# Kernel optimization log

Measured on AMD Instinct MI355X. Metric: run time of the kernel, lower is better.

The kernel has to match this reference:

```python
import jax, jax.numpy as jnp
import numpy as np

B, S, N, IN_D = 16, 12, 2048, 2
H, HEADS, DH = 64, 4, 16
E = 32768
DT = 0.1            # encoder_scale * seq_in / (encoder_interval*seq_in) steps
STEPS = 12          # encoder_interval * seq_in
NEG_SLOPE = 0.2


def setup_inputs() -> dict:
    key = jax.random.key(0)
    ks = jax.random.split(key, 12)
    s = 1.0 / np.sqrt(H)
    return {
        "inputs": jax.random.normal(ks[0], (B, S, N, IN_D), jnp.float32),
        "w_in": jax.random.normal(ks[1], (IN_D, H), jnp.float32) / np.sqrt(IN_D),
        "b_in": jnp.zeros((H,), jnp.float32),
        "Wh": jax.random.normal(ks[2], (H, H), jnp.float32) * s,
        "bias_g": jnp.zeros((H,), jnp.float32),
        "a_src": jax.random.normal(ks[3], (HEADS, DH), jnp.float32) * s,
        "a_dst": jax.random.normal(ks[4], (HEADS, DH), jnp.float32) * s,
        "w1": jax.random.normal(ks[5], (H, H), jnp.float32) * s,
        "b1": jnp.zeros((H,), jnp.float32),
        "w2": jax.random.normal(ks[6], (H, H), jnp.float32) * s,
        "b2": jnp.zeros((H,), jnp.float32),
        "src": jax.random.randint(ks[7], (E,), 0, N, jnp.int32),
        "dst": jax.random.randint(ks[8], (E,), 0, N, jnp.int32),
    }


def _gat(y, Wh, bias_g, a_src, a_dst, src, dst):
    """Single-layer multi-head GAT: dy/dt. y: [B,N,H]."""
    h = (y @ Wh).reshape(B, N, HEADS, DH)                      # [B,N,h,d]
    e_s = jnp.einsum('bnhd,hd->bnh', h, a_src)                 # [B,N,h]
    e_d = jnp.einsum('bnhd,hd->bnh', h, a_dst)
    # per-edge attention logits, leading edge axis for segment ops
    e = jax.nn.leaky_relu(e_s[:, src] + e_d[:, dst], NEG_SLOPE)  # [B,E,h]
    e = jnp.transpose(e, (1, 0, 2))                            # [E,B,h]
    m = jax.ops.segment_max(e, dst, num_segments=N)            # [N,B,h]
    w = jnp.exp(e - m[dst])
    denom = jax.ops.segment_sum(w, dst, num_segments=N)        # [N,B,h]
    alpha = w / denom[dst]                                     # [E,B,h]
    h_src = jnp.transpose(h[:, src], (1, 0, 2, 3))             # [E,B,h,d]
    agg = jax.ops.segment_sum(alpha[..., None] * h_src, dst, num_segments=N)  # [N,B,h,d]
    out = jnp.transpose(agg, (1, 0, 2, 3)).reshape(B, N, H) + bias_g
    return out


def reference(inputs, w_in, b_in, Wh, bias_g, a_src, a_dst, w1, b1, w2, b2, src, dst):
    x = inputs @ w_in + b_in            # [B,S,N,H]
    y0 = x[:, 0]                        # [B,N,H]  (initial state at t=0)

    f = lambda y: _gat(y, Wh, bias_g, a_src, a_dst, src, dst)

    def rk4_step(y, _):
        k1 = f(y)
        k2 = f(y + 0.5 * DT * k1)
        k3 = f(y + 0.5 * DT * k2)
        k4 = f(y + DT * k3)
        y = y + (DT / 6.0) * (k1 + 2.0 * k2 + 2.0 * k3 + k4)
        return y, None

    y, _ = jax.lax.scan(rk4_step, y0, None, length=STEPS)
    out = jnp.tanh(y @ w1 + b1) @ w2 + b2   # output_layer: Linear-Tanh-Linear
    return out
```

## Files before the change

kernel.cpp:

```cpp
#include <hip/hip_runtime.h>

#define NB 16
#define NS 12
#define NN 2048
#define NE 32768
#define NROWS (NB*NN)
#define DTC  0.1f
#define DT2C 0.05f
#define DT6C (0.1f/6.0f)
#define LOG2E 1.44269504088896f
#define CSRCAP 49152


__device__ __forceinline__ unsigned short f2bf(float f) {
    unsigned int u = __float_as_uint(f);
    u = u + 0x7fffu + ((u >> 16) & 1u);
    return (unsigned short)(u >> 16);
}
__device__ __forceinline__ float fexp2(float x) {
#if __has_builtin(__builtin_amdgcn_exp2f)
    return __builtin_amdgcn_exp2f(x);
#else
    return __expf(x * 0.69314718056f);
#endif
}

__global__ __launch_bounds__(256) void init_y_k(const float* __restrict__ inputs,
    const float* __restrict__ w_in, const float* __restrict__ b_in, float* __restrict__ y)
{
    int idx = blockIdx.x * 256 + threadIdx.x;
    int hh = idx & 63;
    int tn = idx >> 6;
    int n = tn >> 4, b = tn & 15;
    const float* ip = inputs + ((size_t)(b * NS) * NN + n) * 2;
    y[idx] = ip[0] * w_in[hh] + ip[1] * w_in[64 + hh] + b_in[hh];
}

__global__ __launch_bounds__(256) void prep_k(int* __restrict__ deg, int* __restrict__ csr,
    float* __restrict__ estA, float* __restrict__ estB)
{
    int t = blockIdx.x * 256 + threadIdx.x;
    if (t < NN) deg[t] = 0;
    if (t < CSRCAP) csr[t] = NN;
    if (t < 64) {
        estA[(size_t)NN * 64 + t] = -1e30f;
        estB[(size_t)NN * 64 + t] = -1e30f;
    }
}
__global__ __launch_bounds__(256) void count_deg_k(const int* __restrict__ dst, int* __restrict__ deg)
{
    int e = blockIdx.x * 256 + threadIdx.x;
    if (e < NE) atomicAdd(&deg[dst[e]], 1);
}
__global__ __launch_bounds__(1024) void scan_k(const int* __restrict__ deg,
    int* __restrict__ offs, int* __restrict__ cursor)
{
    __shared__ int p[1024];
    int t = threadIdx.x;
    int d0 = (deg[2 * t] + 7) & ~7;
    int d1 = (deg[2 * t + 1] + 7) & ~7;
    p[t] = d0 + d1;
    __syncthreads();
    for (int d = 1; d < 1024; d <<= 1) {
        int v = (t >= d) ? p[t - d] : 0;
        __syncthreads();
        p[t] += v;
        __syncthreads();
    }
    int excl = (t > 0) ? p[t - 1] : 0;
    offs[2 * t] = excl;       offs[2 * t + 1] = excl + d0;
    cursor[2 * t] = excl;     cursor[2 * t + 1] = excl + d0;
    if (t == 1023) offs[2048] = p[1023];
}
__global__ __launch_bounds__(256) void scatter_k(const int* __restrict__ src, const int* __restrict__ dst,
    int* __restrict__ cursor, int* __restrict__ csr)
{
    int e = blockIdx.x * 256 + threadIdx.x;
    if (e < NE) {
        int pos = atomicAdd(&cursor[dst[e]], 1);
        csr[pos] = src[e];
    }
}

__global__ __launch_bounds__(1024, 8) void fused_k(
    const float* yin, float* __restrict__ acc, float* yout,
    const uint2* __restrict__ htR, const float* __restrict__ estR, const float* __restrict__ edtR,
    uint2* __restrict__ htW, float* __restrict__ estW, float* __restrict__ edtW,
    const int* __restrict__ offs, const int* __restrict__ csr, const float* __restrict__ bias_g,
    const float* __restrict__ Wh, const float* __restrict__ a_src, const float* __restrict__ a_dst,
    int mode)
{
    __shared__ float kvs[64 * 64];
    __shared__ float Zs[64 * 65];
    __shared__ unsigned int Hs[64 * 33];
    __shared__ float Ps[16][64];
    __shared__ float Pd[16][64];

    int t = threadIdx.x;
    int lane = t & 63;
    int wid = __builtin_amdgcn_readfirstlane(t >> 6);

    if (mode != 0) {
        int np = wid >> 2, bg = wid & 3;
        int n = blockIdx.x * 4 + np;
        int hd = lane >> 4;
        int o0 = offs[n], o1 = offs[n + 1];
        int eoff = bg * 16 + (lane & 15);
        float edv = edtR[(size_t)n * 64 + eoff];
        const uint2* hbase = htR + (size_t)bg * 64 + lane;

        float d0 = 0.f, d1 = 0.f, d2 = 0.f, d3 = 0.f;
        float a0 = 0.f, a1 = 0.f, a2 = 0.f, a3 = 0.f;
        for (int base = o0; base < o1; base += 64) {
            int cnt = o1 - base; if (cnt > 64) cnt = 64;
            int svv = csr[base + (lane < cnt ? lane : cnt - 1)];
            for (int j = 0; j < cnt; j += 8) {
                int ss[8];
                float es8[8];
                uint2 hv8[8];
#pragma unroll
                for (int q = 0; q < 8; q++) ss[q] = __builtin_amdgcn_readlane(svv, j + q);
#pragma unroll
                for (int q = 0; q < 8; q++) es8[q] = estR[(size_t)ss[q] * 64 + eoff];
#pragma unroll
                for (int q = 0; q < 8; q++) hv8[q] = hbase[(size_t)ss[q] * 256];
#pragma unroll
                for (int q = 0; q < 8; q++) {
                    float e = es8[q] + edv;
                    e = fmaxf(e, 0.2f * e);
                    float w = fexp2(e);
                    float w0 = __shfl(w, hd);
                    float w1 = __shfl(w, 4 + hd);
                    float w2 = __shfl(w, 8 + hd);
                    float w3 = __shfl(w, 12 + hd);
                    float h0 = __uint_as_float(hv8[q].x << 16);
                    float h1 = __uint_as_float(hv8[q].x & 0xffff0000u);
                    float h2 = __uint_as_float(hv8[q].y << 16);
                    float h3 = __uint_as_float(hv8[q].y & 0xffff0000u);
                    d0 += w0; a0 += w0 * h0;
                    d1 += w1; a1 += w1 * h1;
                    d2 += w2; a2 += w2 * h2;
                    d3 += w3; a3 += w3 * h3;
                }
            }
        }
        float bgb = bias_g[lane];
        bool has = (o1 > o0);
        float r0 = has ? __builtin_amdgcn_rcpf(d0) : 0.f;
        float r1 = has ? __builtin_amdgcn_rcpf(d1) : 0.f;
        float r2 = has ? __builtin_amdgcn_rcpf(d2) : 0.f;
        float r3 = has ? __builtin_amdgcn_rcpf(d3) : 0.f;
        int rb = np * 16 + bg * 4;
        kvs[(rb + 0) * 64 + lane] = a0 * r0 + bgb;
        kvs[(rb + 1) * 64 + lane] = a1 * r1 + bgb;
        kvs[(rb + 2) * 64 + lane] = a2 * r2 + bgb;
        kvs[(rb + 3) * 64 + lane] = a3 * r3 + bgb;
        __syncthreads();
    }

    int row0 = blockIdx.x * 64;
    const float4* y4 = (const float4*)(yin + (size_t)row0 * 64);
    float4* a4g = (float4*)(acc + (size_t)row0 * 64);
    float4* yo4 = (float4*)(yout + (size_t)row0 * 64);
    int flat = t;
    float4 z = y4[flat];
    if (mode >= 1) {
        float4 kf = *(const float4*)&kvs[flat * 4];
        if (mode == 1) {
            a4g[flat] = kf;
            z.x += DT2C * kf.x; z.y += DT2C * kf.y; z.z += DT2C * kf.z; z.w += DT2C * kf.w;
        } else if (mode == 2) {
            float4 av = a4g[flat];
            av.x += 2.f * kf.x; av.y += 2.f * kf.y; av.z += 2.f * kf.z; av.w += 2.f * kf.w;
            a4g[flat] = av;
            z.x += DT2C * kf.x; z.y += DT2C * kf.y; z.z += DT2C * kf.z; z.w += DT2C * kf.w;
        } else if (mode == 3) {
            float4 av = a4g[flat];
            av.x += 2.f * kf.x; av.y += 2.f * kf.y; av.z += 2.f * kf.z; av.w += 2.f * kf.w;
            a4g[flat] = av;
            z.x += DTC * kf.x; z.y += DTC * kf.y; z.z += DTC * kf.z; z.w += DTC * kf.w;
        } else {
            float4 av = a4g[flat];
            z.x += DT6C * (av.x + kf.x); z.y += DT6C * (av.y + kf.y);
            z.z += DT6C * (av.z + kf.z); z.w += DT6C * (av.w + kf.w);
            yo4[flat] = z;
        }
    }
    if (mode == 5) return;

    {
        int r = flat >> 4;
        int kkb = (flat & 15) << 2;
        Zs[(kkb + 0) * 65 + r] = z.x;
        Zs[(kkb + 1) * 65 + r] = z.y;
        Zs[(kkb + 2) * 65 + r] = z.z;
        Zs[(kkb + 3) * 65 + r] = z.w;
    }
    __syncthreads();

    const float* wcol = Wh + wid * 4;
    float a0 = 0.f, a1 = 0.f, a2 = 0.f, a3 = 0.f;
    for (int kk = 0; kk < 64; kk++) {
        float zk = Zs[kk * 65 + lane];
        const float4* w4 = (const float4*)(wcol + kk * 64);
        float4 w = w4[0];
        a0 += zk * w.x; a1 += zk * w.y; a2 += zk * w.z; a3 += zk * w.w;
    }

    Hs[lane * 33 + wid * 2 + 0] = (unsigned int)f2bf(a0) | ((unsigned int)f2bf(a1) << 16);
    Hs[lane * 33 + wid * 2 + 1] = (unsigned int)f2bf(a2) | ((unsigned int)f2bf(a3) << 16);

    int head = wid >> 2, qp = wid & 3;
    const float* as = a_src + head * 16 + qp * 4;
    const float* ad = a_dst + head * 16 + qp * 4;
    Ps[wid][lane] = a0 * as[0] + a1 * as[1] + a2 * as[2] + a3 * as[3];
    Pd[wid][lane] = a0 * ad[0] + a1 * ad[1] + a2 * ad[2] + a3 * ad[3];
    __syncthreads();

    if (wid < 4) {
        int tn = row0 + lane;
        float sv = (Ps[wid * 4 + 0][lane] + Ps[wid * 4 + 1][lane]
                  + Ps[wid * 4 + 2][lane] + Ps[wid * 4 + 3][lane]) * LOG2E;
        float dv = (Pd[wid * 4 + 0][lane] + Pd[wid * 4 + 1][lane]
                  + Pd[wid * 4 + 2][lane] + Pd[wid * 4 + 3][lane]) * LOG2E;
        estW[(size_t)tn * 4 + wid] = sv;
        edtW[(size_t)tn * 4 + wid] = dv;
    }

    if (t < 512) {
        int nbg = t >> 5;
        int np = nbg >> 2, bg = nbg & 3;
        int cp = t & 31;
        int rbase = np * 16 + bg * 4;
        unsigned int r0 = Hs[(rbase + 0) * 33 + cp];
        unsigned int r1 = Hs[(rbase + 1) * 33 + cp];
        unsigned int r2 = Hs[(rbase + 2) * 33 + cp];
        unsigned int r3 = Hs[(rbase + 3) * 33 + cp];
        uint4 o;
        o.x = (r0 & 0xffffu) | (r1 << 16);
        o.y = (r2 & 0xffffu) | (r3 << 16);
        o.z = (r0 >> 16) | (r1 & 0xffff0000u);
        o.w = (r2 >> 16) | (r3 & 0xffff0000u);
        int ng = blockIdx.x * 4 + np;
        *(uint4*)((unsigned int*)htW + (((size_t)(ng * 4 + bg)) * 64 + 2 * cp) * 2) = o;
    }
}

__global__ __launch_bounds__(256) void mlp_k(
    const float* __restrict__ yin,
    const float* __restrict__ w1, const float* __restrict__ b1,
    const float* __restrict__ w2, const float* __restrict__ b2,
    float* __restrict__ out)
{
    __shared__ float Zs[64 * 65];
    __shared__ float Ts[64 * 65];
    int t = threadIdx.x;
    int row0 = blockIdx.x * 64;
    const float4* y4 = (const float4*)(yin + (size_t)row0 * 64);
#pragma unroll
    for (int i = 0; i < 4; i++) {
        int flat = t + 256 * i;
        float4 z = y4[flat];
        int r = flat >> 4;
        int kkb = (flat & 15) << 2;
        Zs[(kkb + 0) * 65 + r] = z.x;
        Zs[(kkb + 1) * 65 + r] = z.y;
        Zs[(kkb + 2) * 65 + r] = z.z;
        Zs[(kkb + 3) * 65 + r] = z.w;
    }
    __syncthreads();

    int lane = t & 63;
    int g = __builtin_amdgcn_readfirstlane(t >> 6);
    float a[16];
#pragma unroll
    for (int j = 0; j < 16; j++) a[j] = 0.f;
    const float* w1g = w1 + g * 16;
    for (int kk = 0; kk < 64; kk++) {
        float zk = Zs[kk * 65 + lane];
        const float4* w4 = (const float4*)(w1g + kk * 64);
        float4 w0 = w4[0], w1v = w4[1], w2v = w4[2], w3v = w4[3];
        a[0] += zk * w0.x;  a[1] += zk * w0.y;  a[2] += zk * w0.z;  a[3] += zk * w0.w;
        a[4] += zk * w1v.x; a[5] += zk * w1v.y; a[6] += zk * w1v.z; a[7] += zk * w1v.w;
        a[8] += zk * w2v.x; a[9] += zk * w2v.y; a[10] += zk * w2v.z; a[11] += zk * w2v.w;
        a[12] += zk * w3v.x; a[13] += zk * w3v.y; a[14] += zk * w3v.z; a[15] += zk * w3v.w;
    }
    const float4* b1g = (const float4*)(b1 + g * 16);
    float4 bb0 = b1g[0], bb1 = b1g[1], bb2 = b1g[2], bb3 = b1g[3];
    float bb[16] = { bb0.x,bb0.y,bb0.z,bb0.w, bb1.x,bb1.y,bb1.z,bb1.w,
                     bb2.x,bb2.y,bb2.z,bb2.w, bb3.x,bb3.y,bb3.z,bb3.w };
#pragma unroll
    for (int j = 0; j < 16; j++) {
        float v = a[j] + bb[j];
        float ex = __expf(2.f * v);
        float tv = 1.f - 2.f / (ex + 1.f);
        Ts[(16 * g + j) * 65 + lane] = tv;
    }
    __syncthreads();

    float a2[16];
#pragma unroll
    for (int j = 0; j < 16; j++) a2[j] = 0.f;
    const float* w2g = w2 + g * 16;
    for (int kk = 0; kk < 64; kk++) {
        float tk = Ts[kk * 65 + lane];
        const float4* w4 = (const float4*)(w2g + kk * 64);
        float4 w0 = w4[0], w1v = w4[1], w2v = w4[2], w3v = w4[3];
        a2[0] += tk * w0.x;  a2[1] += tk * w0.y;  a2[2] += tk * w0.z;  a2[3] += tk * w0.w;
        a2[4] += tk * w1v.x; a2[5] += tk * w1v.y; a2[6] += tk * w1v.z; a2[7] += tk * w1v.w;
        a2[8] += tk * w2v.x; a2[9] += tk * w2v.y; a2[10] += tk * w2v.z; a2[11] += tk * w2v.w;
        a2[12] += tk * w3v.x; a2[13] += tk * w3v.y; a2[14] += tk * w3v.z; a2[15] += tk * w3v.w;
    }
    const float4* b2g = (const float4*)(b2 + g * 16);
    float4 c0 = b2g[0], c1 = b2g[1], c2 = b2g[2], c3 = b2g[3];
    int tn = row0 + lane;
    int n = tn >> 4, b = tn & 15;
    float4* o4 = (float4*)(out + ((size_t)b * NN + n) * 64 + g * 16);
    o4[0] = make_float4(a2[0] + c0.x, a2[1] + c0.y, a2[2] + c0.z, a2[3] + c0.w);
    o4[1] = make_float4(a2[4] + c1.x, a2[5] + c1.y, a2[6] + c1.z, a2[7] + c1.w);
    o4[2] = make_float4(a2[8] + c2.x, a2[9] + c2.y, a2[10] + c2.z, a2[11] + c2.w);
    o4[3] = make_float4(a2[12] + c3.x, a2[13] + c3.y, a2[14] + c3.z, a2[15] + c3.w);
}

extern "C" void kernel_launch(void* const* d_in, const int* in_sizes, int n_in,
                              void* d_out, int out_size, void* d_ws, size_t ws_size,
                              hipStream_t stream)
{
    const float* inputs = (const float*)d_in[0];
    const float* w_in   = (const float*)d_in[1];
    const float* b_in   = (const float*)d_in[2];
    const float* Wh     = (const float*)d_in[3];
    const float* bias_g = (const float*)d_in[4];
    const float* a_src  = (const float*)d_in[5];
    const float* a_dst  = (const float*)d_in[6];
    const float* w1     = (const float*)d_in[7];
    const float* b1     = (const float*)d_in[8];
    const float* w2     = (const float*)d_in[9];
    const float* b2     = (const float*)d_in[10];
    const int* src      = (const int*)d_in[11];
    const int* dst      = (const int*)d_in[12];
    float* out = (float*)d_out;

    float* ws = (float*)d_ws;
    const size_t SZ = (size_t)NROWS * 64;
    const size_t HTU = 525312;
    const size_t ESF = 131136;
    const size_t EDF = 131072;
    float* y   = ws;
    float* acc = y + SZ;
    uint2* htA = (uint2*)(acc + SZ);
    float* estA = (float*)(htA + HTU);
    float* edtA = estA + ESF;
    uint2* htB = (uint2*)(edtA + EDF);
    float* estB = (float*)(htB + HTU);
    float* edtB = estB + ESF;
    int* offs   = (int*)(edtB + EDF);
    int* cursor = offs + 2064;
    int* deg    = cursor + 2048;
    int* csr    = deg + 2048;

    init_y_k<<<NROWS * 64 / 256, 256, 0, stream>>>(inputs, w_in, b_in, y);
    prep_k<<<CSRCAP / 256, 256, 0, stream>>>(deg, csr, estA, estB);
    count_deg_k<<<NE / 256, 256, 0, stream>>>(dst, deg);
    scan_k<<<1, 1024, 0, stream>>>(deg, offs, cursor);
    scatter_k<<<NE / 256, 256, 0, stream>>>(src, dst, cursor, csr);

    uint2* htR = htA;  float* estR = estA; float* edtR = edtA;
    uint2* htW = htB;  float* estW = estB; float* edtW = edtB;

    fused_k<<<512, 1024, 0, stream>>>(y, acc, y, htB, estB, edtB, htA, estA, edtA,
                                      offs, csr, bias_g, Wh, a_src, a_dst, 0);
    for (int step = 0; step < 12; step++) {
        for (int st = 1; st <= 4; st++) {
            int mode = (step == 11 && st == 4) ? 5 : st;
            fused_k<<<512, 1024, 0, stream>>>(y, acc, y, htR, estR, edtR, htW, estW, edtW,
                                              offs, csr, bias_g, Wh, a_src, a_dst, mode);
            uint2* th = htR; htR = htW; htW = th;
            float* te = estR; estR = estW; estW = te;
            float* td = edtR; edtR = edtW; edtW = td;
        }
    }
    mlp_k<<<512, 256, 0, stream>>>(y, w1, b1, w2, b2, out);
}
```

Baseline: 1.071 ms.

## Replace per-stage launches with one persistent cooperative kernel using grid sync

The 49 separate launches of the fused GAT/RK4 stage kernel become a single cooperative persistent kernel with 256 blocks, each covering 128 rows in two passes, separated by grid.sync(). The RK4 state y and the accumulator now stay in registers across stages rather than going through global memory, and the initial projection is folded into the kernel. This removes launch overhead and the global y/acc traffic. In exchange there are only 256 blocks of 1024 threads (half the previous parallelism, each doing twice the work), grid-wide barriers, and a smaller edge-loop unroll, which may hurt latency hiding.

```diff
diff --git a/kernel.cpp b/kernel.cpp
--- a/kernel.cpp
+++ b/kernel.cpp
@@ -1,4 +1,5 @@
 #include <hip/hip_runtime.h>
+#include <hip/hip_cooperative_groups.h>
 
 #define NB 16
 #define NS 12
@@ -23,17 +24,6 @@
 #else
     return __expf(x * 0.69314718056f);
 #endif
-}
-
-__global__ __launch_bounds__(256) void init_y_k(const float* __restrict__ inputs,
-    const float* __restrict__ w_in, const float* __restrict__ b_in, float* __restrict__ y)
-{
-    int idx = blockIdx.x * 256 + threadIdx.x;
-    int hh = idx & 63;
-    int tn = idx >> 6;
-    int n = tn >> 4, b = tn & 15;
-    const float* ip = inputs + ((size_t)(b * NS) * NN + n) * 2;
-    y[idx] = ip[0] * w_in[hh] + ip[1] * w_in[64 + hh] + b_in[hh];
 }
 
 __global__ __launch_bounds__(256) void prep_k(int* __restrict__ deg, int* __restrict__ csr,
@@ -82,13 +72,13 @@
     }
 }
 
-__global__ __launch_bounds__(1024, 8) void fused_k(
-    const float* yin, float* __restrict__ acc, float* yout,
-    const uint2* __restrict__ htR, const float* __restrict__ estR, const float* __restrict__ edtR,
-    uint2* __restrict__ htW, float* __restrict__ estW, float* __restrict__ edtW,
+__global__ __launch_bounds__(1024, 4) void persist_k(
+    const float* __restrict__ inputs, const float* __restrict__ w_in, const float* __restrict__ b_in,
+    uint2* __restrict__ htA, float* __restrict__ estA, float* __restrict__ edtA,
+    uint2* __restrict__ htB, float* __restrict__ estB, float* __restrict__ edtB,
     const int* __restrict__ offs, const int* __restrict__ csr, const float* __restrict__ bias_g,
     const float* __restrict__ Wh, const float* __restrict__ a_src, const float* __restrict__ a_dst,
-    int mode)
+    float* __restrict__ yout)
 {
     __shared__ float kvs[64 * 64];
     __shared__ float Zs[64 * 65];
@@ -96,153 +86,188 @@
     __shared__ float Ps[16][64];
     __shared__ float Pd[16][64];
 
+    cooperative_groups::grid_group grid = cooperative_groups::this_grid();
+
     int t = threadIdx.x;
     int lane = t & 63;
     int wid = __builtin_amdgcn_readfirstlane(t >> 6);
-
-    if (mode != 0) {
-        int np = wid >> 2, bg = wid & 3;
-        int n = blockIdx.x * 4 + np;
-        int hd = lane >> 4;
-        int o0 = offs[n], o1 = offs[n + 1];
-        int eoff = bg * 16 + (lane & 15);
-        float edv = edtR[(size_t)n * 64 + eoff];
-        const uint2* hbase = htR + (size_t)bg * 64 + lane;
-
-        float d0 = 0.f, d1 = 0.f, d2 = 0.f, d3 = 0.f;
-        float a0 = 0.f, a1 = 0.f, a2 = 0.f, a3 = 0.f;
-        for (int base = o0; base < o1; base += 64) {
-            int cnt = o1 - base; if (cnt > 64) cnt = 64;
-            int svv = csr[base + (lane < cnt ? lane : cnt - 1)];
-            for (int j = 0; j < cnt; j += 8) {
-                int ss[8];
-                float es8[8];
-                uint2 hv8[8];
-#pragma unroll
-                for (int q = 0; q < 8; q++) ss[q] = __builtin_amdgcn_readlane(svv, j + q);
-#pragma unroll
-                for (int q = 0; q < 8; q++) es8[q] = estR[(size_t)ss[q] * 64 + eoff];
-#pragma unroll
-                for (int q = 0; q < 8; q++) hv8[q] = hbase[(size_t)ss[q] * 256];
-#pragma unroll
-                for (int q = 0; q < 8; q++) {
-                    float e = es8[q] + edv;
-                    e = fmaxf(e, 0.2f * e);
-                    float w = fexp2(e);
-                    float w0 = __shfl(w, hd);
-                    float w1 = __shfl(w, 4 + hd);
-                    float w2 = __shfl(w, 8 + hd);
-                    float w3 = __shfl(w, 12 + hd);
-                    float h0 = __uint_as_float(hv8[q].x << 16);
-                    float h1 = __uint_as_float(hv8[q].x & 0xffff0000u);
-                    float h2 = __uint_as_float(hv8[q].y << 16);
-                    float h3 = __uint_as_float(hv8[q].y & 0xffff0000u);
-                    d0 += w0; a0 += w0 * h0;
-                    d1 += w1; a1 += w1 * h1;
-                    d2 += w2; a2 += w2 * h2;
-                    d3 += w3; a3 += w3 * h3;
+    int row0 = blockIdx.x * 128;
+
+    float4 yr[2], accr[2];
+#pragma unroll
+    for (int p = 0; p < 2; p++) {
+        int r = t >> 4, q = t & 15;
+        int tn = row0 + p * 64 + r;
+        int n0 = tn >> 4, b0 = tn & 15;
+        const float* ip = inputs + ((size_t)(b0 * NS) * NN + n0) * 2;
+        float i0 = ip[0], i1 = ip[1];
+        float4 wa = ((const float4*)w_in)[q];
+        float4 wb = ((const float4*)(w_in + 64))[q];
+        float4 bb = ((const float4*)b_in)[q];
+        yr[p].x = i0 * wa.x + i1 * wb.x + bb.x;
+        yr[p].y = i0 * wa.y + i1 * wb.y + bb.y;
+        yr[p].z = i0 * wa.z + i1 * wb.z + bb.z;
+        yr[p].w = i0 * wa.w + i1 * wb.w + bb.w;
+        accr[p] = make_float4(0.f, 0.f, 0.f, 0.f);
+    }
+
+    for (int ev = 0; ev <= 48; ev++) {
+        int mode = (ev == 0) ? 0 : ((ev - 1) & 3) + 1;
+        bool last = (ev == 48);
+        const uint2* htR; const float* estR; const float* edtR;
+        uint2* htW; float* estW; float* edtW;
+        if (ev & 1) { htR = htA; estR = estA; edtR = edtA; htW = htB; estW = estB; edtW = edtB; }
+        else        { htR = htB; estR = estB; edtR = edtB; htW = htA; estW = estA; edtW = edtA; }
+
+#pragma unroll
+        for (int p = 0; p < 2; p++) {
+            if (mode != 0) {
+                int np = wid >> 2, bg = wid & 3;
+                int n = blockIdx.x * 8 + p * 4 + np;
+                int hd = lane >> 4;
+                int o0 = offs[n], o1 = offs[n + 1];
+                int eoff = bg * 16 + (lane & 15);
+                float edv = edtR[(size_t)n * 64 + eoff];
+                const uint2* hbase = htR + (size_t)bg * 64 + lane;
+
+                float d0 = 0.f, d1 = 0.f, d2 = 0.f, d3 = 0.f;
+                float a0 = 0.f, a1 = 0.f, a2 = 0.f, a3 = 0.f;
+                for (int base = o0; base < o1; base += 64) {
+                    int cnt = o1 - base; if (cnt > 64) cnt = 64;
+                    int svv = csr[base + (lane < cnt ? lane : cnt - 1)];
+                    for (int j = 0; j < cnt; j += 4) {
+                        int ss[4]; float es4[4]; uint2 hv4[4];
+#pragma unroll
+                        for (int qq = 0; qq < 4; qq++) ss[qq] = __builtin_amdgcn_readlane(svv, j + qq);
+#pragma unroll
+                        for (int qq = 0; qq < 4; qq++) es4[qq] = estR[(size_t)ss[qq] * 64 + eoff];
+#pragma unroll
+                        for (int qq = 0; qq < 4; qq++) hv4[qq] = hbase[(size_t)ss[qq] * 256];
+#pragma unroll
+                        for (int qq = 0; qq < 4; qq++) {
+                            float e = es4[qq] + edv;
+                            e = fmaxf(e, 0.2f * e);
+                            float w = fexp2(e);
+                            float w0 = __shfl(w, hd);
+                            float w1 = __shfl(w, 4 + hd);
+                            float w2 = __shfl(w, 8 + hd);
+                            float w3 = __shfl(w, 12 + hd);
+                            float h0 = __uint_as_float(hv4[qq].x << 16);
+                            float h1 = __uint_as_float(hv4[qq].x & 0xffff0000u);
+                            float h2 = __uint_as_float(hv4[qq].y << 16);
+                            float h3 = __uint_as_float(hv4[qq].y & 0xffff0000u);
+                            d0 += w0; a0 += w0 * h0;
+                            d1 += w1; a1 += w1 * h1;
+                            d2 += w2; a2 += w2 * h2;
+                            d3 += w3; a3 += w3 * h3;
+                        }
+                    }
                 }
-            }
+                float bgb = bias_g[lane];
+                bool has = (o1 > o0);
+                float r0 = has ? __builtin_amdgcn_rcpf(d0) : 0.f;
+                float r1 = has ? __builtin_amdgcn_rcpf(d1) : 0.f;
+                float r2 = has ? __builtin_amdgcn_rcpf(d2) : 0.f;
+                float r3 = has ? __builtin_amdgcn_rcpf(d3) : 0.f;
+                int rb = np * 16 + bg * 4;
+                kvs[(rb + 0) * 64 + lane] = a0 * r0 + bgb;
+                kvs[(rb + 1) * 64 + lane] = a1 * r1 + bgb;
+                kvs[(rb + 2) * 64 + lane] = a2 * r2 + bgb;
+                kvs[(rb + 3) * 64 + lane] = a3 * r3 + bgb;
+                __syncthreads();
+            }
+
+            float4 z = yr[p];
+            if (mode >= 1) {
+                float4 kf = *(const float4*)&kvs[t * 4];
+                if (mode == 1) {
+                    accr[p] = kf;
+                    z.x += DT2C * kf.x; z.y += DT2C * kf.y; z.z += DT2C * kf.z; z.w += DT2C * kf.w;
+                } else if (mode == 2) {
+                    accr[p].x += 2.f * kf.x; accr[p].y += 2.f * kf.y;
+                    accr[p].z += 2.f * kf.z; accr[p].w += 2.f * kf.w;
+                    z.x += DT2C * kf.x; z.y += DT2C * kf.y; z.z += DT2C * kf.z; z.w += DT2C * kf.w;
+                } else if (mode == 3) {
+                    accr[p].x += 2.f * kf.x; accr[p].y += 2.f * kf.y;
+                    accr[p].z += 2.f * kf.z; accr[p].w += 2.f * kf.w;
+                    z.x += DTC * kf.x; z.y += DTC * kf.y; z.z += DTC * kf.z; z.w += DTC * kf.w;
+                } else {
+                    yr[p].x += DT6C * (accr[p].x + kf.x); yr[p].y += DT6C * (accr[p].y + kf.y);
+                    yr[p].z += DT6C * (accr[p].z + kf.z); yr[p].w += DT6C * (accr[p].w + kf.w);
+                    z = yr[p];
+                }
+            }
+            if (last) {
+                __syncthreads();
+                continue;
+            }
+
+            {
+                int rr = t >> 4;
+                int kkb = (t & 15) << 2;
+                Zs[(kkb + 0) * 65 + rr] = z.x;
+                Zs[(kkb + 1) * 65 + rr] = z.y;
+                Zs[(kkb + 2) * 65 + rr] = z.z;
+                Zs[(kkb + 3) * 65 + rr] = z.w;
+            }
+            __syncthreads();
+
+            const float* wcol = Wh + wid * 4;
+            float a0 = 0.f, a1 = 0.f, a2 = 0.f, a3 = 0.f;
+            for (int kk = 0; kk < 64; kk++) {
+                float zk = Zs[kk * 65 + lane];
+                float4 w = *(const float4*)(wcol + kk * 64);
+                a0 += zk * w.x; a1 += zk * w.y; a2 += zk * w.z; a3 += zk * w.w;
+            }
+
+            Hs[lane * 33 + wid * 2 + 0] = (unsigned int)f2bf(a0) | ((unsigned int)f2bf(a1) << 16);
+            Hs[lane * 33 + wid * 2 + 1] = (unsigned int)f2bf(a2) | ((unsigned int)f2bf(a3) << 16);
+
+            int head = wid >> 2, qp = wid & 3;
+            const float* as = a_src + head * 16 + qp * 4;
+            const float* ad = a_dst + head * 16 + qp * 4;
+            Ps[wid][lane] = a0 * as[0] + a1 * as[1] + a2 * as[2] + a3 * as[3];
+            Pd[wid][lane] = a0 * ad[0] + a1 * ad[1] + a2 * ad[2] + a3 * ad[3];
+            __syncthreads();
+
+            if (wid < 4) {
+                int tn2 = row0 + p * 64 + lane;
+                float sv = (Ps[wid * 4 + 0][lane] + Ps[wid * 4 + 1][lane]
+                          + Ps[wid * 4 + 2][lane] + Ps[wid * 4 + 3][lane]) * LOG2E;
+                float dv = (Pd[wid * 4 + 0][lane] + Pd[wid * 4 + 1][lane]
+                          + Pd[wid * 4 + 2][lane] + Pd[wid * 4 + 3][lane]) * LOG2E;
+                estW[(size_t)tn2 * 4 + wid] = sv;
+                edtW[(size_t)tn2 * 4 + wid] = dv;
+            }
+
+            if (t < 512) {
+                int nbg = t >> 5;
+                int np2 = nbg >> 2, bg2 = nbg & 3;
+                int cp = t & 31;
+                int rbase = np2 * 16 + bg2 * 4;
+                unsigned int r0 = Hs[(rbase + 0) * 33 + cp];
+                unsigned int r1 = Hs[(rbase + 1) * 33 + cp];
+                unsigned int r2 = Hs[(rbase + 2) * 33 + cp];
+                unsigned int r3 = Hs[(rbase + 3) * 33 + cp];
+                uint4 o;
+                o.x = (r0 & 0xffffu) | (r1 << 16);
+                o.y = (r2 & 0xffffu) | (r3 << 16);
+                o.z = (r0 >> 16) | (r1 & 0xffff0000u);
+                o.w = (r2 >> 16) | (r3 & 0xffff0000u);
+                int ng = blockIdx.x * 8 + p * 4 + np2;
+                *(uint4*)((unsigned int*)htW + (((size_t)(ng * 4 + bg2)) * 64 + 2 * cp) * 2) = o;
+            }
+            __syncthreads();
         }
-        float bgb = bias_g[lane];
-        bool has = (o1 > o0);
-        float r0 = has ? __builtin_amdgcn_rcpf(d0) : 0.f;
-        float r1 = has ? __builtin_amdgcn_rcpf(d1) : 0.f;
-        float r2 = has ? __builtin_amdgcn_rcpf(d2) : 0.f;
-        float r3 = has ? __builtin_amdgcn_rcpf(d3) : 0.f;
-        int rb = np * 16 + bg * 4;
-        kvs[(rb + 0) * 64 + lane] = a0 * r0 + bgb;
-        kvs[(rb + 1) * 64 + lane] = a1 * r1 + bgb;
-        kvs[(rb + 2) * 64 + lane] = a2 * r2 + bgb;
-        kvs[(rb + 3) * 64 + lane] = a3 * r3 + bgb;
-        __syncthreads();
-    }
-
-    int row0 = blockIdx.x * 64;
-    const float4* y4 = (const float4*)(yin + (size_t)row0 * 64);
-    float4* a4g = (float4*)(acc + (size_t)row0 * 64);
-    float4* yo4 = (float4*)(yout + (size_t)row0 * 64);
-    int flat = t;
-    float4 z = y4[flat];
-    if (mode >= 1) {
-        float4 kf = *(const float4*)&kvs[flat * 4];
-        if (mode == 1) {
-            a4g[flat] = kf;
-            z.x += DT2C * kf.x; z.y += DT2C * kf.y; z.z += DT2C * kf.z; z.w += DT2C * kf.w;
-        } else if (mode == 2) {
-            float4 av = a4g[flat];
-            av.x += 2.f * kf.x; av.y += 2.f * kf.y; av.z += 2.f * kf.z; av.w += 2.f * kf.w;
-            a4g[flat] = av;
-            z.x += DT2C * kf.x; z.y += DT2C * kf.y; z.z += DT2C * kf.z; z.w += DT2C * kf.w;
-        } else if (mode == 3) {
-            float4 av = a4g[flat];
-            av.x += 2.f * kf.x; av.y += 2.f * kf.y; av.z += 2.f * kf.z; av.w += 2.f * kf.w;
-            a4g[flat] = av;
-            z.x += DTC * kf.x; z.y += DTC * kf.y; z.z += DTC * kf.z; z.w += DTC * kf.w;
-        } else {
-            float4 av = a4g[flat];
-            z.x += DT6C * (av.x + kf.x); z.y += DT6C * (av.y + kf.y);
-            z.z += DT6C * (av.z + kf.z); z.w += DT6C * (av.w + kf.w);
-            yo4[flat] = z;
-        }
-    }
-    if (mode == 5) return;
-
-    {
-        int r = flat >> 4;
-        int kkb = (flat & 15) << 2;
-        Zs[(kkb + 0) * 65 + r] = z.x;
-        Zs[(kkb + 1) * 65 + r] = z.y;
-        Zs[(kkb + 2) * 65 + r] = z.z;
-        Zs[(kkb + 3) * 65 + r] = z.w;
-    }
-    __syncthreads();
-
-    const float* wcol = Wh + wid * 4;
-    float a0 = 0.f, a1 = 0.f, a2 = 0.f, a3 = 0.f;
-    for (int kk = 0; kk < 64; kk++) {
-        float zk = Zs[kk * 65 + lane];
-        const float4* w4 = (const float4*)(wcol + kk * 64);
-        float4 w = w4[0];
-        a0 += zk * w.x; a1 += zk * w.y; a2 += zk * w.z; a3 += zk * w.w;
-    }
-
-    Hs[lane * 33 + wid * 2 + 0] = (unsigned int)f2bf(a0) | ((unsigned int)f2bf(a1) << 16);
-    Hs[lane * 33 + wid * 2 + 1] = (unsigned int)f2bf(a2) | ((unsigned int)f2bf(a3) << 16);
-
-    int head = wid >> 2, qp = wid & 3;
-    const float* as = a_src + head * 16 + qp * 4;
-    const float* ad = a_dst + head * 16 + qp * 4;
-    Ps[wid][lane] = a0 * as[0] + a1 * as[1] + a2 * as[2] + a3 * as[3];
-    Pd[wid][lane] = a0 * ad[0] + a1 * ad[1] + a2 * ad[2] + a3 * ad[3];
-    __syncthreads();
-
-    if (wid < 4) {
-        int tn = row0 + lane;
-        float sv = (Ps[wid * 4 + 0][lane] + Ps[wid * 4 + 1][lane]
-                  + Ps[wid * 4 + 2][lane] + Ps[wid * 4 + 3][lane]) * LOG2E;
-        float dv = (Pd[wid * 4 + 0][lane] + Pd[wid * 4 + 1][lane]
-                  + Pd[wid * 4 + 2][lane] + Pd[wid * 4 + 3][lane]) * LOG2E;
-        estW[(size_t)tn * 4 + wid] = sv;
-        edtW[(size_t)tn * 4 + wid] = dv;
-    }
-
-    if (t < 512) {
-        int nbg = t >> 5;
-        int np = nbg >> 2, bg = nbg & 3;
-        int cp = t & 31;
-        int rbase = np * 16 + bg * 4;
-        unsigned int r0 = Hs[(rbase + 0) * 33 + cp];
-        unsigned int r1 = Hs[(rbase + 1) * 33 + cp];
-        unsigned int r2 = Hs[(rbase + 2) * 33 + cp];
-        unsigned int r3 = Hs[(rbase + 3) * 33 + cp];
-        uint4 o;
-        o.x = (r0 & 0xffffu) | (r1 << 16);
-        o.y = (r2 & 0xffffu) | (r3 << 16);
-        o.z = (r0 >> 16) | (r1 & 0xffff0000u);
-        o.w = (r2 >> 16) | (r3 & 0xffff0000u);
-        int ng = blockIdx.x * 4 + np;
-        *(uint4*)((unsigned int*)htW + (((size_t)(ng * 4 + bg)) * 64 + 2 * cp) * 2) = o;
+
+        if (last) break;
+        grid.sync();
+    }
+
+#pragma unroll
+    for (int p = 0; p < 2; p++) {
+        float4* yo4 = (float4*)(yout + (size_t)(row0 + p * 64) * 64);
+        yo4[t] = yr[p];
     }
 }
 
@@ -347,8 +372,7 @@
     const size_t ESF = 131136;
     const size_t EDF = 131072;
     float* y   = ws;
-    float* acc = y + SZ;
-    uint2* htA = (uint2*)(acc + SZ);
+    uint2* htA = (uint2*)(y + SZ);
     float* estA = (float*)(htA + HTU);
     float* edtA = estA + ESF;
     uint2* htB = (uint2*)(edtA + EDF);
@@ -359,26 +383,20 @@
     int* deg    = cursor + 2048;
     int* csr    = deg + 2048;
 
-    init_y_k<<<NROWS * 64 / 256, 256, 0, stream>>>(inputs, w_in, b_in, y);
     prep_k<<<CSRCAP / 256, 256, 0, stream>>>(deg, csr, estA, estB);
     count_deg_k<<<NE / 256, 256, 0, stream>>>(dst, deg);
     scan_k<<<1, 1024, 0, stream>>>(deg, offs, cursor);
     scatter_k<<<NE / 256, 256, 0, stream>>>(src, dst, cursor, csr);
 
-    uint2* htR = htA;  float* estR = estA; float* edtR = edtA;
-    uint2* htW = htB;  float* estW = estB; float* edtW = edtB;
-
-    fused_k<<<512, 1024, 0, stream>>>(y, acc, y, htB, estB, edtB, htA, estA, edtA,
-                                      offs, csr, bias_g, Wh, a_src, a_dst, 0);
-    for (int step = 0; step < 12; step++) {
-        for (int st = 1; st <= 4; st++) {
-            int mode = (step == 11 && st == 4) ? 5 : st;
-            fused_k<<<512, 1024, 0, stream>>>(y, acc, y, htR, estR, edtR, htW, estW, edtW,
-                                              offs, csr, bias_g, Wh, a_src, a_dst, mode);
-            uint2* th = htR; htR = htW; htW = th;
-            float* te = estR; estR = estW; estW = te;
-            float* td = edtR; edtR = edtW; edtW = td;
-        }
-    }
+    void* args[] = {
+        (void*)&inputs, (void*)&w_in, (void*)&b_in,
+        (void*)&htA, (void*)&estA, (void*)&edtA,
+        (void*)&htB, (void*)&estB, (void*)&edtB,
+        (void*)&offs, (void*)&csr, (void*)&bias_g,
+        (void*)&Wh, (void*)&a_src, (void*)&a_dst,
+        (void*)&y
+    };
+    hipLaunchCooperativeKernel((void*)persist_k, dim3(256), dim3(1024), args, 0, stream);
+
     mlp_k<<<512, 256, 0, stream>>>(y, w1, b1, w2, b2, out);
 }
```

Result: slower. 2.463 ms (+130.0%).
